# Kernel optimization log

Hardware: AMD Instinct MI355X
Metric: run time of the kernel (lower is better)

The kernel has to match this reference:

```python
import jax, jax.numpy as jnp
import numpy as np

S = 1024          # num tokens (single prefill sequence)
H = 2880          # hidden_size
NH = 64           # num query heads
NKV = 8           # num kv heads
HD = 64           # head_dim
G = NH // NKV     # query heads per kv head
THETA = 10000.0
SCALE = HD ** -0.5


def _rope(x, positions):
    # neox-style rotary over full head_dim; x: [S, n_heads, HD]
    half = HD // 2
    inv_freq = 1.0 / (THETA ** (jnp.arange(half, dtype=jnp.float32) / half))
    ang = positions.astype(jnp.float32)[:, None] * inv_freq          # [S, half]
    cos = jnp.cos(ang)[:, None, :]
    sin = jnp.sin(ang)[:, None, :]
    x1, x2 = x[..., :half], x[..., half:]
    return jnp.concatenate([x1 * cos - x2 * sin, x2 * cos + x1 * sin], axis=-1)


def setup_inputs() -> dict:
    key = jax.random.key(0)
    k0, k1, k2, k3 = jax.random.split(key, 4)
    return {
        "positions": jnp.arange(S, dtype=jnp.int32),
        "hidden_states": jax.random.normal(k0, (S, H), dtype=jnp.float32),
        "qkv_w": jax.random.normal(k1, ((NH + 2 * NKV) * HD, H), dtype=jnp.float32) * 0.02,
        "o_w": jax.random.normal(k2, (H, NH * HD), dtype=jnp.float32) * 0.02,
        "sinks": jax.random.normal(k3, (NH,), dtype=jnp.float32),
    }


def reference(positions, hidden_states, qkv_w, o_w, sinks):
    # fused QKV projection (no bias, matching attention_bias=False)
    qkv = hidden_states @ qkv_w.T                                     # [S, 5120]
    q = qkv[:, : NH * HD].reshape(S, NH, HD)
    k = qkv[:, NH * HD : NH * HD + NKV * HD].reshape(S, NKV, HD)
    v = qkv[:, NH * HD + NKV * HD :].reshape(S, NKV, HD)

    # rotary on q and k (rotary_dim == head_dim)
    q = _rope(q, positions)
    k = _rope(k, positions)

    # GQA: group query heads by kv head -> [S, NKV, G, HD]
    qg = q.reshape(S, NKV, G, HD)

    logits = jnp.einsum("qghd,kgd->ghqk", qg, k) * SCALE              # [NKV, G, S, S]
    causal = positions[:, None] >= positions[None, :]                 # [S, S]
    logits = jnp.where(causal[None, None], logits, -jnp.inf)

    # attention sinks: per-head extra logit in the softmax denominator,
    # contributing no value vector.
    sink = sinks.reshape(NKV, G)[:, :, None, None]                    # [NKV, G, 1, 1]
    m = jnp.maximum(jnp.max(logits, axis=-1, keepdims=True), sink)
    p = jnp.exp(logits - m)                                           # [NKV, G, S, S]
    denom = jnp.sum(p, axis=-1, keepdims=True) + jnp.exp(sink - m)
    attn = jnp.einsum("ghqk,kgd->qghd", p / denom, v)                 # [S, NKV, G, HD]

    out = attn.reshape(S, NH * HD) @ o_w.T                            # [S, H]
    return out
```

## Files before the change

### kernel.cpp

```cpp
#include <hip/hip_runtime.h>
#include <hip/hip_bf16.h>
#include <math.h>

#define S_LEN 1024
#define HDIM  2880
#define NH    64
#define NKV   8
#define HD    64
#define QKV_N ((NH + 2*NKV) * HD)
#define O_K   (NH * HD)
#define SCALE 0.125f

typedef _Float16 f16x8 __attribute__((ext_vector_type(8)));
typedef _Float16 f16x4 __attribute__((ext_vector_type(4)));
typedef float    f32x4 __attribute__((ext_vector_type(4)));

__global__ __launch_bounds__(256) void cvt_f32_f16(const float* __restrict__ src,
                                                   _Float16* __restrict__ dst, int n4) {
    const int stride = gridDim.x * blockDim.x;
    for (int i = blockIdx.x * blockDim.x + threadIdx.x; i < n4; i += stride) {
        const float4 v = ((const float4*)src)[i];
        f16x4 p;
        p[0] = (_Float16)v.x; p[1] = (_Float16)v.y;
        p[2] = (_Float16)v.z; p[3] = (_Float16)v.w;
        ((f16x4*)dst)[i] = p;
    }
}

#define CSTR 68
template<typename CT>
__global__ __launch_bounds__(256) void gemm_f16(const _Float16* __restrict__ A,
                                                const float* __restrict__ B,
                                                CT* __restrict__ C,
                                                int M, int N, int K) {
    __shared__ __align__(16) _Float16 sh[128 * CSTR];
    _Float16* As = sh;
    _Float16* Bs = sh + 4096;

    const int tid  = threadIdx.x;
    const int lane = tid & 63;
    const int wave = tid >> 6;
    const int wr   = wave >> 1;
    const int wc   = wave & 1;
    const int quad = lane >> 4;
    const int fr   = lane & 15;
    const int ks   = quad * 8;
    const int row0 = blockIdx.y * 128;
    const int col0 = blockIdx.x * 128;

    const int klen = K / (int)gridDim.z;
    const int kb   = (int)blockIdx.z * klen;
    CT* Cp = C + (size_t)blockIdx.z * M * N;

    f32x4 acc[4][4] = {};

    for (int k0 = kb; k0 < kb + klen; k0 += 32) {
        __syncthreads();
#pragma unroll
        for (int it = 0; it < 2; ++it) {
            const int cbase = it * 256 + wave * 64;
            const int ci = cbase + lane;
            const int r  = ci >> 2;
            const int ch = ci & 3;
            const _Float16* gp = A + (size_t)(row0 + r) * K + k0 + ch * 8;
            __builtin_amdgcn_global_load_lds(
                (const __attribute__((address_space(1))) void*)gp,
                (__attribute__((address_space(3))) void*)(As + (size_t)cbase * 8),
                16, 0, 0);
        }
#pragma unroll
        for (int it = 0; it < 4; ++it) {
            const int c4 = it * 256 + tid;
            const int r  = c4 >> 3;
            const int ch = (c4 & 7) << 2;
            int brow = col0 + r;
            if (brow >= N) brow = N - 1;
            const float4 bv = *(const float4*)&B[(size_t)brow * K + k0 + ch];
            f16x4 p;
            p[0] = (_Float16)bv.x; p[1] = (_Float16)bv.y;
            p[2] = (_Float16)bv.z; p[3] = (_Float16)bv.w;
            *(f16x4*)&Bs[r * 32 + ch] = p;
        }
        __syncthreads();

        f16x8 af[4], bfr[4];
#pragma unroll
        for (int mi = 0; mi < 4; ++mi)
            af[mi] = *(const f16x8*)&As[(wr * 64 + mi * 16 + fr) * 32 + ks];
#pragma unroll
        for (int ni = 0; ni < 4; ++ni)
            bfr[ni] = *(const f16x8*)&Bs[(wc * 64 + ni * 16 + fr) * 32 + ks];
#pragma unroll
        for (int mi = 0; mi < 4; ++mi)
#pragma unroll
            for (int ni = 0; ni < 4; ++ni)
                acc[mi][ni] = __builtin_amdgcn_mfma_f32_16x16x32_f16(
                    af[mi], bfr[ni], acc[mi][ni], 0, 0, 0);
    }

#pragma unroll
    for (int p = 0; p < 2; ++p) {
        __syncthreads();
        if (wc == p) {
#pragma unroll
            for (int mi = 0; mi < 4; ++mi)
#pragma unroll
                for (int ni = 0; ni < 4; ++ni) {
                    const f32x4 v = acc[mi][ni];
#pragma unroll
                    for (int r = 0; r < 4; ++r)
                        sh[(wr * 64 + mi * 16 + quad * 4 + r) * CSTR + ni * 16 + fr] =
                            (_Float16)v[r];
                }
        }
        __syncthreads();
#pragma unroll
        for (int it = 0; it < 4; ++it) {
            const int id  = it * 256 + tid;
            const int row = id >> 3;
            const int ch  = (id & 7) * 8;
            const int col = col0 + p * 64 + ch;
            if (col < N) {
                const f16x4 lo = *(const f16x4*)&sh[row * CSTR + ch];
                const f16x4 hi = *(const f16x4*)&sh[row * CSTR + ch + 4];
                if constexpr (sizeof(CT) == 2) {
                    f16x8 v;
                    v[0]=lo[0]; v[1]=lo[1]; v[2]=lo[2]; v[3]=lo[3];
                    v[4]=hi[0]; v[5]=hi[1]; v[6]=hi[2]; v[7]=hi[3];
                    *(f16x8*)&Cp[(size_t)(row0 + row) * N + col] = v;
                } else {
                    float4 v0 = make_float4((float)lo[0], (float)lo[1],
                                            (float)lo[2], (float)lo[3]);
                    float4 v1 = make_float4((float)hi[0], (float)hi[1],
                                            (float)hi[2], (float)hi[3]);
                    *(float4*)&Cp[(size_t)(row0 + row) * N + col]     = v0;
                    *(float4*)&Cp[(size_t)(row0 + row) * N + col + 4] = v1;
                }
            }
        }
    }
}

__global__ __launch_bounds__(256) void rope_reduce(_Float16* __restrict__ parts,
                                                   int nsplit,
                                                   _Float16* __restrict__ vt,
                                                   const int* __restrict__ positions) {
    __shared__ float buf[QKV_N];
    const int s   = blockIdx.x;
    const int tid = threadIdx.x;
    const size_t PSTR = (size_t)S_LEN * QKV_N;

    for (int c = tid; c < QKV_N / 4; c += 256) {
        float4 a = make_float4(0.f, 0.f, 0.f, 0.f);
        for (int j = 0; j < nsplit; ++j) {
            const f16x4 v = ((const f16x4*)(parts + j * PSTR + (size_t)s * QKV_N))[c];
            a.x += (float)v[0]; a.y += (float)v[1];
            a.z += (float)v[2]; a.w += (float)v[3];
        }
        ((float4*)buf)[c] = a;
    }
    __syncthreads();

    const float pos = (float)positions[s];
    _Float16* orow = parts + (size_t)s * QKV_N;
    for (int w = tid; w < 72 * 32; w += 256) {
        const int h = w >> 5;
        const int t = w & 31;
        const float inv_freq = exp2f(-(float)t * (13.287712379549449f / 32.0f));
        const float ang = pos * inv_freq;
        float sn, cs;
        sincosf(ang, &sn, &cs);
        const float x1 = buf[h * 64 + t];
        const float x2 = buf[h * 64 + t + 32];
        orow[h * 64 + t]      = (_Float16)(x1 * cs - x2 * sn);
        orow[h * 64 + t + 32] = (_Float16)(x2 * cs + x1 * sn);
    }
    for (int c = tid; c < NKV * HD; c += 256)
        vt[(size_t)c * S_LEN + s] = (_Float16)buf[(NH + NKV) * HD + c];
}

__global__ __launch_bounds__(256) void o_reduce(const _Float16* __restrict__ parts,
                                                float* __restrict__ out,
                                                int n4, int nsplit) {
    const size_t PSTR = (size_t)S_LEN * HDIM;
    const int stride = gridDim.x * blockDim.x;
    for (int i = blockIdx.x * blockDim.x + threadIdx.x; i < n4; i += stride) {
        float4 a = make_float4(0.f, 0.f, 0.f, 0.f);
        for (int j = 0; j < nsplit; ++j) {
            const f16x4 v = ((const f16x4*)(parts + j * PSTR))[i];
            a.x += (float)v[0]; a.y += (float)v[1];
            a.z += (float)v[2]; a.w += (float)v[3];
        }
        ((float4*)out)[i] = a;
    }
}

#define LSTR 72
__global__ __launch_bounds__(256) void attn_mfma(const _Float16* __restrict__ qkv,
                                                 const _Float16* __restrict__ vt,
                                                 const float* __restrict__ sinks,
                                                 const int* __restrict__ positions,
                                                 _Float16* __restrict__ attn_out) {
    __shared__ __align__(16) _Float16 Ks[64 * LSTR];
    __shared__ __align__(16) _Float16 Vs[64 * LSTR];
    __shared__ __align__(16) _Float16 Ps[64 * LSTR];
    __shared__ int posk[64];

    const int tid  = threadIdx.x;
    const int lane = tid & 63;
    const int wave = tid >> 6;
    const int fr   = lane & 15;
    const int quad = lane >> 4;
    const int ks8  = quad * 8;
    const int n    = blockIdx.x;
    const int qt   = (int)gridDim.y - 1 - (int)blockIdx.y;
    const int g    = n >> 3;

    const _Float16* qrow = qkv + (size_t)(qt * 64 + wave * 16 + fr) * QKV_N + n * HD;
    const f16x8 a_q0 = *(const f16x8*)&qrow[ks8];
    const f16x8 a_q1 = *(const f16x8*)&qrow[32 + ks8];

    int pq[4];
#pragma unroll
    for (int r = 0; r < 4; ++r)
        pq[r] = positions[qt * 64 + wave * 16 + quad * 4 + r];

    const float sinkv = sinks[n];
    float m[4], l[4];
    f32x4 o[4] = {};
#pragma unroll
    for (int r = 0; r < 4; ++r) { m[r] = sinkv; l[r] = 1.0f; }

    for (int kt = 0; kt <= qt; ++kt) {
        __syncthreads();
        const _Float16* Kg = qkv + (size_t)(kt * 64) * QKV_N + NH * HD + g * HD;
        const _Float16* Vg = vt + (size_t)(g * HD) * S_LEN + kt * 64;
#pragma unroll
        for (int it = 0; it < 2; ++it) {
            const int c = it * 256 + tid;
            const int r = c >> 3, off8 = (c & 7) * 8;
            const f16x8 kv = *(const f16x8*)&Kg[(size_t)r * QKV_N + off8];
            *(f16x8*)&Ks[r * LSTR + off8] = kv;
            const f16x8 vv = *(const f16x8*)&Vg[(size_t)r * S_LEN + off8];
            *(f16x8*)&Vs[r * LSTR + off8] = vv;
        }
        if (tid < 64) posk[tid] = positions[kt * 64 + tid];
        __syncthreads();

        f32x4 s[4] = {};
#pragma unroll
        for (int nt = 0; nt < 4; ++nt) {
            const f16x8 b0 = *(const f16x8*)&Ks[(nt * 16 + fr) * LSTR + ks8];
            s[nt] = __builtin_amdgcn_mfma_f32_16x16x32_f16(a_q0, b0, s[nt], 0, 0, 0);
            const f16x8 b1 = *(const f16x8*)&Ks[(nt * 16 + fr) * LSTR + 32 + ks8];
            s[nt] = __builtin_amdgcn_mfma_f32_16x16x32_f16(a_q1, b1, s[nt], 0, 0, 0);
        }

        const bool diag = (kt == qt);
        int pk[4];
        if (diag) {
#pragma unroll
            for (int nt = 0; nt < 4; ++nt) pk[nt] = posk[nt * 16 + fr];
        }
#pragma unroll
        for (int nt = 0; nt < 4; ++nt)
#pragma unroll
            for (int r = 0; r < 4; ++r) {
                float sv = s[nt][r] * SCALE;
                if (diag && pk[nt] > pq[r]) sv = -3.0e38f;
                s[nt][r] = sv;
            }

#pragma unroll
        for (int r = 0; r < 4; ++r) {
            float tm = fmaxf(fmaxf(s[0][r], s[1][r]), fmaxf(s[2][r], s[3][r]));
            tm = fmaxf(tm, __shfl_xor(tm, 1, 64));
            tm = fmaxf(tm, __shfl_xor(tm, 2, 64));
            tm = fmaxf(tm, __shfl_xor(tm, 4, 64));
            tm = fmaxf(tm, __shfl_xor(tm, 8, 64));
            const float nm = fmaxf(m[r], tm);
            const float alpha = __expf(m[r] - nm);
            float rs = 0.0f;
#pragma unroll
            for (int nt = 0; nt < 4; ++nt) {
                const float p = __expf(s[nt][r] - nm);
                s[nt][r] = p;
                rs += p;
            }
            rs += __shfl_xor(rs, 1, 64);
            rs += __shfl_xor(rs, 2, 64);
            rs += __shfl_xor(rs, 4, 64);
            rs += __shfl_xor(rs, 8, 64);
            l[r] = l[r] * alpha + rs;
            m[r] = nm;
#pragma unroll
            for (int nt = 0; nt < 4; ++nt) o[nt][r] *= alpha;
        }

#pragma unroll
        for (int nt = 0; nt < 4; ++nt)
#pragma unroll
            for (int r = 0; r < 4; ++r)
                Ps[(wave * 16 + quad * 4 + r) * LSTR + nt * 16 + fr] = (_Float16)s[nt][r];
        __threadfence_block();

#pragma unroll
        for (int k2 = 0; k2 < 2; ++k2) {
            const f16x8 ap = *(const f16x8*)&Ps[(wave * 16 + fr) * LSTR + k2 * 32 + ks8];
#pragma unroll
            for (int nt = 0; nt < 4; ++nt) {
                const f16x8 bv = *(const f16x8*)&Vs[(nt * 16 + fr) * LSTR + k2 * 32 + ks8];
                o[nt] = __builtin_amdgcn_mfma_f32_16x16x32_f16(ap, bv, o[nt], 0, 0, 0);
            }
        }
    }

#pragma unroll
    for (int r = 0; r < 4; ++r) {
        const float inv = 1.0f / l[r];
        const size_t row = (size_t)(qt * 64 + wave * 16 + quad * 4 + r);
#pragma unroll
        for (int nt = 0; nt < 4; ++nt)
            attn_out[row * O_K + n * HD + nt * 16 + fr] = (_Float16)(o[nt][r] * inv);
    }
}

extern "C" void kernel_launch(void* const* d_in, const int* in_sizes, int n_in,
                              void* d_out, int out_size, void* d_ws, size_t ws_size,
                              hipStream_t stream) {
    const int*   positions = (const int*)d_in[0];
    const float* hidden    = (const float*)d_in[1];
    const float* qkv_w     = (const float*)d_in[2];
    const float* o_w       = (const float*)d_in[3];
    const float* sinks     = (const float*)d_in[4];
    float* out = (float*)d_out;

    const size_t n_hid  = (size_t)S_LEN * HDIM;
    const size_t n_qkv  = (size_t)S_LEN * QKV_N;
    const size_t n_attn = (size_t)S_LEN * O_K;
    const size_t n_vt   = (size_t)NKV * HD * S_LEN;
    const size_t n_out  = (size_t)S_LEN * HDIM;

    const int SP_Q = 6;
    const int SP_O = 8;

    const size_t need = (n_hid + SP_Q * n_qkv + n_attn + n_vt) * sizeof(_Float16);

    if (ws_size >= need) {
        _Float16* hid_h  = (_Float16*)d_ws;
        _Float16* qkvp   = hid_h + n_hid;
        _Float16* attn_h = qkvp + SP_Q * n_qkv;
        _Float16* vt     = attn_h + n_attn;
        _Float16* opart  = qkvp;

        cvt_f32_f16<<<512, 256, 0, stream>>>(hidden, hid_h, (int)(n_hid / 4));
        gemm_f16<_Float16><<<dim3(QKV_N / 128, S_LEN / 128, SP_Q), 256, 0, stream>>>(
            hid_h, qkv_w, qkvp, S_LEN, QKV_N, HDIM);
        rope_reduce<<<S_LEN, 256, 0, stream>>>(qkvp, SP_Q, vt, positions);
        attn_mfma<<<dim3(NH, S_LEN / 64), 256, 0, stream>>>(qkvp, vt, sinks, positions, attn_h);
        gemm_f16<_Float16><<<dim3((HDIM + 127) / 128, S_LEN / 128, SP_O), 256, 0, stream>>>(
            attn_h, o_w, opart, S_LEN, HDIM, O_K);
        o_reduce<<<1024, 256, 0, stream>>>(opart, out, (int)(n_out / 4), SP_O);
    } else {
        _Float16* hid_h  = (_Float16*)d_ws;
        _Float16* qkvp   = hid_h + n_hid;
        _Float16* attn_h = qkvp + n_qkv;
        _Float16* vt     = attn_h + n_attn;

        cvt_f32_f16<<<512, 256, 0, stream>>>(hidden, hid_h, (int)(n_hid / 4));
        gemm_f16<_Float16><<<dim3(QKV_N / 128, S_LEN / 128, 1), 256, 0, stream>>>(
            hid_h, qkv_w, qkvp, S_LEN, QKV_N, HDIM);
        rope_reduce<<<S_LEN, 256, 0, stream>>>(qkvp, 1, vt, positions);
        attn_mfma<<<dim3(NH, S_LEN / 64), 256, 0, stream>>>(qkvp, vt, sinks, positions, attn_h);
        gemm_f16<float><<<dim3((HDIM + 127) / 128, S_LEN / 128, 1), 256, 0, stream>>>(
            attn_h, o_w, out, S_LEN, HDIM, O_K);
    }
}
```

Measured before the change: 331.0 us.

## Double-buffer LDS tiles in GEMM and attention, halve split-K factors

The fp16 GEMM now uses two LDS buffers for its A and B tiles. It issues the next K-step's async A loads and B register loads before the MFMA work on the current tile, and writes the converted B tile to the other buffer afterwards, so one barrier per step replaces two. The attention kernel likewise prefetches the next K/V tile into registers during compute and stores it into a second LDS buffer, and it reads diagonal key positions straight from global memory instead of a shared array. Split-K factors for the QKV and output projections are halved, which cuts partial-sum traffic and reduction work but gives fewer blocks and longer K loops per block. Doubled LDS use may lower occupancy.

```diff
diff --git a/kernel.cpp b/kernel.cpp
--- a/kernel.cpp
+++ b/kernel.cpp
@@ -33,9 +33,7 @@
                                                 const float* __restrict__ B,
                                                 CT* __restrict__ C,
                                                 int M, int N, int K) {
-    __shared__ __align__(16) _Float16 sh[128 * CSTR];
-    _Float16* As = sh;
-    _Float16* Bs = sh + 4096;
+    __shared__ __align__(16) _Float16 sh[16384];
 
     const int tid  = threadIdx.x;
     const int lane = tid & 63;
@@ -48,54 +46,105 @@
     const int row0 = blockIdx.y * 128;
     const int col0 = blockIdx.x * 128;
 
-    const int klen = K / (int)gridDim.z;
-    const int kb   = (int)blockIdx.z * klen;
+    const int klen   = K / (int)gridDim.z;
+    const int kb     = (int)blockIdx.z * klen;
+    const int nsteps = klen / 32;
     CT* Cp = C + (size_t)blockIdx.z * M * N;
 
+    const int a_cbase0 = wave * 64;
+    const int a_ci0 = a_cbase0 + lane;
+    const int a_r0 = a_ci0 >> 2, a_ch0 = a_ci0 & 3;
+    const int a_cbase1 = 256 + wave * 64;
+    const int a_ci1 = a_cbase1 + lane;
+    const int a_r1 = a_ci1 >> 2, a_ch1 = a_ci1 & 3;
+    int b_r[4], b_ch[4];
+#pragma unroll
+    for (int it = 0; it < 4; ++it) {
+        const int c4 = it * 256 + tid;
+        b_r[it]  = c4 >> 3;
+        b_ch[it] = (c4 & 7) << 2;
+    }
+
+    float4 breg[4];
     f32x4 acc[4][4] = {};
 
-    for (int k0 = kb; k0 < kb + klen; k0 += 32) {
+    {
+        const _Float16* gp0 = A + (size_t)(row0 + a_r0) * K + kb + a_ch0 * 8;
+        __builtin_amdgcn_global_load_lds(
+            (const __attribute__((address_space(1))) void*)gp0,
+            (__attribute__((address_space(3))) void*)(sh + (size_t)a_cbase0 * 8), 16, 0, 0);
+        const _Float16* gp1 = A + (size_t)(row0 + a_r1) * K + kb + a_ch1 * 8;
+        __builtin_amdgcn_global_load_lds(
+            (const __attribute__((address_space(1))) void*)gp1,
+            (__attribute__((address_space(3))) void*)(sh + (size_t)a_cbase1 * 8), 16, 0, 0);
+#pragma unroll
+        for (int it = 0; it < 4; ++it) {
+            int brow = col0 + b_r[it];
+            if (brow >= N) brow = N - 1;
+            breg[it] = *(const float4*)&B[(size_t)brow * K + kb + b_ch[it]];
+        }
+        _Float16* Bs0 = sh + 8192;
+#pragma unroll
+        for (int it = 0; it < 4; ++it) {
+            f16x4 p;
+            p[0] = (_Float16)breg[it].x; p[1] = (_Float16)breg[it].y;
+            p[2] = (_Float16)breg[it].z; p[3] = (_Float16)breg[it].w;
+            *(f16x4*)&Bs0[b_r[it] * 32 + b_ch[it]] = p;
+        }
+    }
+
+    for (int step = 0; step < nsteps; ++step) {
+        const int cur = step & 1;
+        const int nxt = cur ^ 1;
+        _Float16* Acur = sh + cur * 4096;
+        _Float16* Anxt = sh + nxt * 4096;
+        _Float16* Bcur = sh + 8192 + cur * 4096;
+        _Float16* Bnxt = sh + 8192 + nxt * 4096;
+
         __syncthreads();
-#pragma unroll
-        for (int it = 0; it < 2; ++it) {
-            const int cbase = it * 256 + wave * 64;
-            const int ci = cbase + lane;
-            const int r  = ci >> 2;
-            const int ch = ci & 3;
-            const _Float16* gp = A + (size_t)(row0 + r) * K + k0 + ch * 8;
+
+        const bool more = (step + 1 < nsteps);
+        if (more) {
+            const int k1 = kb + (step + 1) * 32;
+            const _Float16* gp0 = A + (size_t)(row0 + a_r0) * K + k1 + a_ch0 * 8;
             __builtin_amdgcn_global_load_lds(
-                (const __attribute__((address_space(1))) void*)gp,
-                (__attribute__((address_space(3))) void*)(As + (size_t)cbase * 8),
-                16, 0, 0);
-        }
-#pragma unroll
-        for (int it = 0; it < 4; ++it) {
-            const int c4 = it * 256 + tid;
-            const int r  = c4 >> 3;
-            const int ch = (c4 & 7) << 2;
-            int brow = col0 + r;
-            if (brow >= N) brow = N - 1;
-            const float4 bv = *(const float4*)&B[(size_t)brow * K + k0 + ch];
-            f16x4 p;
-            p[0] = (_Float16)bv.x; p[1] = (_Float16)bv.y;
-            p[2] = (_Float16)bv.z; p[3] = (_Float16)bv.w;
-            *(f16x4*)&Bs[r * 32 + ch] = p;
-        }
-        __syncthreads();
+                (const __attribute__((address_space(1))) void*)gp0,
+                (__attribute__((address_space(3))) void*)(Anxt + (size_t)a_cbase0 * 8), 16, 0, 0);
+            const _Float16* gp1 = A + (size_t)(row0 + a_r1) * K + k1 + a_ch1 * 8;
+            __builtin_amdgcn_global_load_lds(
+                (const __attribute__((address_space(1))) void*)gp1,
+                (__attribute__((address_space(3))) void*)(Anxt + (size_t)a_cbase1 * 8), 16, 0, 0);
+#pragma unroll
+            for (int it = 0; it < 4; ++it) {
+                int brow = col0 + b_r[it];
+                if (brow >= N) brow = N - 1;
+                breg[it] = *(const float4*)&B[(size_t)brow * K + k1 + b_ch[it]];
+            }
+        }
 
         f16x8 af[4], bfr[4];
 #pragma unroll
         for (int mi = 0; mi < 4; ++mi)
-            af[mi] = *(const f16x8*)&As[(wr * 64 + mi * 16 + fr) * 32 + ks];
+            af[mi] = *(const f16x8*)&Acur[(wr * 64 + mi * 16 + fr) * 32 + ks];
 #pragma unroll
         for (int ni = 0; ni < 4; ++ni)
-            bfr[ni] = *(const f16x8*)&Bs[(wc * 64 + ni * 16 + fr) * 32 + ks];
+            bfr[ni] = *(const f16x8*)&Bcur[(wc * 64 + ni * 16 + fr) * 32 + ks];
 #pragma unroll
         for (int mi = 0; mi < 4; ++mi)
 #pragma unroll
             for (int ni = 0; ni < 4; ++ni)
                 acc[mi][ni] = __builtin_amdgcn_mfma_f32_16x16x32_f16(
                     af[mi], bfr[ni], acc[mi][ni], 0, 0, 0);
+
+        if (more) {
+#pragma unroll
+            for (int it = 0; it < 4; ++it) {
+                f16x4 p;
+                p[0] = (_Float16)breg[it].x; p[1] = (_Float16)breg[it].y;
+                p[2] = (_Float16)breg[it].z; p[3] = (_Float16)breg[it].w;
+                *(f16x4*)&Bnxt[b_r[it] * 32 + b_ch[it]] = p;
+            }
+        }
     }
 
 #pragma unroll
@@ -201,10 +250,9 @@
                                                  const float* __restrict__ sinks,
                                                  const int* __restrict__ positions,
                                                  _Float16* __restrict__ attn_out) {
-    __shared__ __align__(16) _Float16 Ks[64 * LSTR];
-    __shared__ __align__(16) _Float16 Vs[64 * LSTR];
+    __shared__ __align__(16) _Float16 Ks[2][64 * LSTR];
+    __shared__ __align__(16) _Float16 Vs[2][64 * LSTR];
     __shared__ __align__(16) _Float16 Ps[64 * LSTR];
-    __shared__ int posk[64];
 
     const int tid  = threadIdx.x;
     const int lane = tid & 63;
@@ -216,6 +264,14 @@
     const int qt   = (int)gridDim.y - 1 - (int)blockIdx.y;
     const int g    = n >> 3;
 
+    int st_r[2], st_o[2];
+#pragma unroll
+    for (int it = 0; it < 2; ++it) {
+        const int c = it * 256 + tid;
+        st_r[it] = c >> 3;
+        st_o[it] = (c & 7) * 8;
+    }
+
     const _Float16* qrow = qkv + (size_t)(qt * 64 + wave * 16 + fr) * QKV_N + n * HD;
     const f16x8 a_q0 = *(const f16x8*)&qrow[ks8];
     const f16x8 a_q1 = *(const f16x8*)&qrow[32 + ks8];
@@ -231,28 +287,44 @@
 #pragma unroll
     for (int r = 0; r < 4; ++r) { m[r] = sinkv; l[r] = 1.0f; }
 
+    f16x8 kreg[2], vreg[2];
+    {
+        const _Float16* Kg = qkv + (size_t)0 * QKV_N + NH * HD + g * HD;
+        const _Float16* Vg = vt + (size_t)(g * HD) * S_LEN;
+#pragma unroll
+        for (int it = 0; it < 2; ++it) {
+            kreg[it] = *(const f16x8*)&Kg[(size_t)st_r[it] * QKV_N + st_o[it]];
+            vreg[it] = *(const f16x8*)&Vg[(size_t)st_r[it] * S_LEN + st_o[it]];
+        }
+#pragma unroll
+        for (int it = 0; it < 2; ++it) {
+            *(f16x8*)&Ks[0][st_r[it] * LSTR + st_o[it]] = kreg[it];
+            *(f16x8*)&Vs[0][st_r[it] * LSTR + st_o[it]] = vreg[it];
+        }
+    }
+
     for (int kt = 0; kt <= qt; ++kt) {
+        const int cur = kt & 1;
+        const int nxt = cur ^ 1;
         __syncthreads();
-        const _Float16* Kg = qkv + (size_t)(kt * 64) * QKV_N + NH * HD + g * HD;
-        const _Float16* Vg = vt + (size_t)(g * HD) * S_LEN + kt * 64;
-#pragma unroll
-        for (int it = 0; it < 2; ++it) {
-            const int c = it * 256 + tid;
-            const int r = c >> 3, off8 = (c & 7) * 8;
-            const f16x8 kv = *(const f16x8*)&Kg[(size_t)r * QKV_N + off8];
-            *(f16x8*)&Ks[r * LSTR + off8] = kv;
-            const f16x8 vv = *(const f16x8*)&Vg[(size_t)r * S_LEN + off8];
-            *(f16x8*)&Vs[r * LSTR + off8] = vv;
-        }
-        if (tid < 64) posk[tid] = positions[kt * 64 + tid];
-        __syncthreads();
+
+        const bool more = (kt < qt);
+        if (more) {
+            const _Float16* Kg = qkv + (size_t)((kt + 1) * 64) * QKV_N + NH * HD + g * HD;
+            const _Float16* Vg = vt + (size_t)(g * HD) * S_LEN + (kt + 1) * 64;
+#pragma unroll
+            for (int it = 0; it < 2; ++it) {
+                kreg[it] = *(const f16x8*)&Kg[(size_t)st_r[it] * QKV_N + st_o[it]];
+                vreg[it] = *(const f16x8*)&Vg[(size_t)st_r[it] * S_LEN + st_o[it]];
+            }
+        }
 
         f32x4 s[4] = {};
 #pragma unroll
         for (int nt = 0; nt < 4; ++nt) {
-            const f16x8 b0 = *(const f16x8*)&Ks[(nt * 16 + fr) * LSTR + ks8];
+            const f16x8 b0 = *(const f16x8*)&Ks[cur][(nt * 16 + fr) * LSTR + ks8];
             s[nt] = __builtin_amdgcn_mfma_f32_16x16x32_f16(a_q0, b0, s[nt], 0, 0, 0);
-            const f16x8 b1 = *(const f16x8*)&Ks[(nt * 16 + fr) * LSTR + 32 + ks8];
+            const f16x8 b1 = *(const f16x8*)&Ks[cur][(nt * 16 + fr) * LSTR + 32 + ks8];
             s[nt] = __builtin_amdgcn_mfma_f32_16x16x32_f16(a_q1, b1, s[nt], 0, 0, 0);
         }
 
@@ -260,7 +332,7 @@
         int pk[4];
         if (diag) {
 #pragma unroll
-            for (int nt = 0; nt < 4; ++nt) pk[nt] = posk[nt * 16 + fr];
+            for (int nt = 0; nt < 4; ++nt) pk[nt] = positions[qt * 64 + nt * 16 + fr];
         }
 #pragma unroll
         for (int nt = 0; nt < 4; ++nt)
@@ -309,8 +381,16 @@
             const f16x8 ap = *(const f16x8*)&Ps[(wave * 16 + fr) * LSTR + k2 * 32 + ks8];
 #pragma unroll
             for (int nt = 0; nt < 4; ++nt) {
-                const f16x8 bv = *(const f16x8*)&Vs[(nt * 16 + fr) * LSTR + k2 * 32 + ks8];
+                const f16x8 bv = *(const f16x8*)&Vs[cur][(nt * 16 + fr) * LSTR + k2 * 32 + ks8];
                 o[nt] = __builtin_amdgcn_mfma_f32_16x16x32_f16(ap, bv, o[nt], 0, 0, 0);
+            }
+        }
+
+        if (more) {
+#pragma unroll
+            for (int it = 0; it < 2; ++it) {
+                *(f16x8*)&Ks[nxt][st_r[it] * LSTR + st_o[it]] = kreg[it];
+                *(f16x8*)&Vs[nxt][st_r[it] * LSTR + st_o[it]] = vreg[it];
             }
         }
     }
@@ -341,8 +421,8 @@
     const size_t n_vt   = (size_t)NKV * HD * S_LEN;
     const size_t n_out  = (size_t)S_LEN * HDIM;
 
-    const int SP_Q = 6;
-    const int SP_O = 8;
+    const int SP_Q = 3;
+    const int SP_O = 4;
 
     const size_t need = (n_hid + SP_Q * n_qkv + n_attn + n_vt) * sizeof(_Float16);
 
```

New measurement: 304.6 us. 8.0% less time.
